# Kernel optimization log

Measured on AMD Instinct MI355X. Metric: run time of the kernel, lower is better.

## Reference

```python
import jax, jax.numpy as jnp
import numpy as np

B, D, N, H = 2, 1024, 2048, 16
DH = D // H  # head dim 64


def setup_inputs() -> dict:
    key = jax.random.key(0)
    ks = jax.random.split(key, 10)
    query = jax.random.normal(ks[0], (B, D, N), jnp.float32)
    att_mask = jax.random.randint(ks[1], (B, 1, N), 0, 2).astype(bool)
    w = lambda k: jax.random.normal(k, (D, D), jnp.float32) * 0.02
    b = lambda k: jax.random.normal(k, (D,), jnp.float32) * 0.02
    return dict(
        query=query,
        Wq=w(ks[2]), bq=b(ks[3]),
        Wk=w(ks[4]), bk=b(ks[5]),
        Wv=w(ks[6]), bv=b(ks[7]),
        Wo=w(ks[8]), bo=b(ks[9]),
        att_mask=att_mask,
    )


def _proj(W, bias, x):  # conv1d k=1: [B,D,N] -> [B,D,N]
    return jnp.einsum('ed,bdn->ben', W, x) + bias[None, :, None]


def _split_heads(t):  # [B,N,D] -> [B*H,N,DH], batch-major flatten
    return t.reshape(B, N, H, DH).transpose(0, 2, 1, 3).reshape(B * H, N, DH)


def _attention(q, k, v, att_mask):
    scale = 1.0 / np.sqrt(DH)
    att = jnp.einsum('bqd,bkd->bqk', q * scale, k)  # [B*H,N,N]
    # faithful to original: mask repeated along q_len then tiled num_heads times on dim 0
    m = jnp.tile(jnp.broadcast_to(att_mask, (B, N, N)), (H, 1, 1))
    att = jnp.where(m, att, -jnp.inf)
    fully_masked = ~m.any(axis=(-2, -1))  # [B*H]
    att = jnp.where(fully_masked[:, None, None], 1e-5, att)
    p = jax.nn.softmax(att, axis=-1)
    y = jnp.einsum('bqk,bkd->bqd', p, v)
    return y * (~fully_masked).astype(y.dtype)[:, None, None]


def reference(query, Wq, bq, Wk, bk, Wv, bv, Wo, bo, att_mask):
    # projections (Conv1d kernel_size=1 == channel-dim linear)
    q = _split_heads(_proj(Wq, bq, query).transpose(0, 2, 1))
    k = _split_heads(_proj(Wk, bk, query).transpose(0, 2, 1))
    v = _split_heads(_proj(Wv, bv, query).transpose(0, 2, 1))
    y = _attention(q, k, v, att_mask)  # [B*H,N,DH]
    # combine heads -> [B,N,D] -> channels-first [B,D,N]
    z = y.reshape(B, H, N, DH).transpose(0, 2, 1, 3).reshape(B, N, D).transpose(0, 2, 1)
    # output projection (dropouts are identity in eval mode)
    return _proj(Wo, bo, z)
```

## Files before the change

kernel.cpp:

```cpp
#include <hip/hip_runtime.h>
#include <hip/hip_bf16.h>

#define BATCH 2
#define DMODEL 1024
#define SEQ 2048
#define NHEAD 16
#define DHEAD 64
#define BH (BATCH*NHEAD)
#define COLS (BATCH*SEQ)

typedef __attribute__((ext_vector_type(8))) short bf16x8;
typedef __attribute__((ext_vector_type(4))) float f32x4;
typedef __attribute__((ext_vector_type(16))) float f32x16;

__device__ inline unsigned short f2bf(float f) {
    unsigned u = __builtin_bit_cast(unsigned, f);
    unsigned r = (u + 0x7FFFu + ((u >> 16) & 1u)) >> 16;
    return (unsigned short)r;
}

__device__ inline f32x4 mfma16(bf16x8 a, bf16x8 b, f32x4 c) {
    return __builtin_amdgcn_mfma_f32_16x16x32_bf16(a, b, c, 0, 0, 0);
}
__device__ inline f32x16 mfma32(bf16x8 a, bf16x8 b, f32x16 c) {
    return __builtin_amdgcn_mfma_f32_32x32x16_bf16(a, b, c, 0, 0, 0);
}

__device__ __forceinline__ void gload_lds16(const unsigned short* g, unsigned short* l) {
    __builtin_amdgcn_global_load_lds(
        (const __attribute__((address_space(1))) unsigned int*)g,
        (__attribute__((address_space(3))) unsigned int*)l, 16, 0, 0);
}

__device__ inline unsigned cvtpk(float lo, float hi) {
    unsigned r;
    asm("v_cvt_pk_bf16_f32 %0, %1, %2" : "=v"(r) : "v"(lo), "v"(hi));
    return r;
}
__device__ inline float fexp2(float x) {
    float r;
    asm("v_exp_f32 %0, %1" : "=v"(r) : "v"(x));
    return r;
}

__global__ __launch_bounds__(256) void cvt_w(
    const float* __restrict__ w0, const float* __restrict__ w1,
    const float* __restrict__ w2, const float* __restrict__ w3,
    unsigned short* __restrict__ out)
{
    int which = blockIdx.y;
    const float* src = (which == 0) ? w0 : (which == 1) ? w1 : (which == 2) ? w2 : w3;
    size_t base = (size_t)which * (DMODEL * DMODEL);
    size_t i = ((size_t)blockIdx.x * 256 + threadIdx.x) * 4;
    float4 v = *(const float4*)&src[i];
    ushort4 o;
    o.x = f2bf(v.x); o.y = f2bf(v.y); o.z = f2bf(v.z); o.w = f2bf(v.w);
    *(ushort4*)&out[base + i] = o;
}

__global__ __launch_bounds__(64) void prep_mask(
    const int* __restrict__ mask, unsigned long long* __restrict__ mw)
{
    int lane = threadIdx.x;
    int tile = blockIdx.x;
    int mb = tile >> 5, tt = tile & 31;
    unsigned long long bits = __ballot(mask[mb * SEQ + tt * 64 + lane] != 0);
    if (lane == 0) mw[tile] = bits;
}

__global__ __launch_bounds__(256) void transpose_q(
    const float* __restrict__ q, unsigned short* __restrict__ Xt)
{
    __shared__ float tile[32][33];
    int b = blockIdx.z;
    int d0 = blockIdx.y * 32, n0 = blockIdx.x * 32;
    int tx = threadIdx.x, ty = threadIdx.y;
#pragma unroll
    for (int i = 0; i < 32; i += 8)
        tile[ty + i][tx] = q[(size_t)b * DMODEL * SEQ + (size_t)(d0 + ty + i) * SEQ + n0 + tx];
    __syncthreads();
#pragma unroll
    for (int i = 0; i < 32; i += 8)
        Xt[(size_t)b * SEQ * DMODEL + (size_t)(n0 + ty + i) * DMODEL + d0 + tx] = f2bf(tile[tx][ty + i]);
}

__global__ __launch_bounds__(256) void gemm_qkv(
    const unsigned short* __restrict__ Xt,
    const unsigned short* __restrict__ W3,
    const float* __restrict__ bq, const float* __restrict__ bk, const float* __restrict__ bv,
    unsigned short* __restrict__ Qb, unsigned short* __restrict__ Kbuf,
    unsigned short* __restrict__ Vtb)
{
    const int K = DMODEL;
    __shared__ unsigned short sA[128 * 32];
    __shared__ unsigned short sB[128 * 32];
    int t = threadIdx.x, lane = t & 63, w = t >> 6;
    int wr = w >> 1, wc = w & 1;
    int tt0 = blockIdx.y * 128;
    int ct0 = blockIdx.x * 128;
    int mat = ct0 >> 10, ec0 = ct0 & 1023;
    const float* bs = (mat == 0) ? bq : (mat == 1) ? bk : bv;
    int rl = lane & 15, ko = (lane >> 4) << 3;
    int srow = lane >> 2, scol = (lane & 3) << 3;

    f32x4 acc[4][4] = {};
    for (int kb = 0; kb < K; kb += 32) {
        __syncthreads();
        gload_lds16(&Xt[(size_t)(tt0 + w * 32 + srow) * K + kb + scol],      &sA[(w * 32) * 32]);
        gload_lds16(&Xt[(size_t)(tt0 + w * 32 + 16 + srow) * K + kb + scol], &sA[(w * 32 + 16) * 32]);
        gload_lds16(&W3[(size_t)(ct0 + w * 32 + srow) * K + kb + scol],      &sB[(w * 32) * 32]);
        gload_lds16(&W3[(size_t)(ct0 + w * 32 + 16 + srow) * K + kb + scol], &sB[(w * 32 + 16) * 32]);
        __syncthreads();
        bf16x8 af[4], bfr[4];
#pragma unroll
        for (int m = 0; m < 4; m++)
            af[m] = *(const bf16x8*)&sA[(wr * 64 + m * 16 + rl) * 32 + ko];
#pragma unroll
        for (int n = 0; n < 4; n++)
            bfr[n] = *(const bf16x8*)&sB[(wc * 64 + n * 16 + rl) * 32 + ko];
#pragma unroll
        for (int m = 0; m < 4; m++)
#pragma unroll
            for (int n = 0; n < 4; n++)
                acc[m][n] = mfma16(af[m], bfr[n], acc[m][n]);
    }

    const float QS = 0.125f;
    int rowb = (lane >> 4) * 4, col = lane & 15;
#pragma unroll
    for (int m = 0; m < 4; m++) {
#pragma unroll
        for (int n = 0; n < 4; n++) {
            int ee = ec0 + wc * 64 + n * 16 + col;
            int hh = ee >> 6, dd = ee & 63;
            float bias = bs[ee];
#pragma unroll
            for (int r = 0; r < 4; r++) {
                int tk = tt0 + wr * 64 + m * 16 + rowb + r;
                int b = tk >> 11, nn = tk & (SEQ - 1);
                float v = acc[m][n][r] + bias;
                if (mat == 0) {
                    v *= QS;
                    Qb[((size_t)(b * NHEAD + hh) * SEQ + nn) * DHEAD + dd] = f2bf(v);
                } else if (mat == 1) {
                    Kbuf[((size_t)(b * NHEAD + hh) * SEQ + nn) * DHEAD + dd] = f2bf(v);
                } else {
                    int q2 = (nn >> 2) & 3;
                    int q2s = ((q2 & 1) << 1) | (q2 >> 1);
                    int np = (nn & ~15) | (q2s << 2) | (nn & 3);
                    Vtb[((size_t)(b * NHEAD + hh) * DHEAD + dd) * SEQ + np] = f2bf(v);
                }
            }
        }
    }
}

__global__ __launch_bounds__(256) void gemm_out(
    const unsigned short* __restrict__ A,
    const unsigned short* __restrict__ Bt,
    const float* __restrict__ bias,
    float* __restrict__ outf)
{
    const int K = DMODEL;
    __shared__ unsigned short sA[128 * 32];
    __shared__ unsigned short sB[64 * 32];
    int t = threadIdx.x, lane = t & 63, w = t >> 6;
    int wr = w >> 1, wc = w & 1;
    int et0 = blockIdx.y * 128, ct0 = blockIdx.x * 64;
    int rl = lane & 15, ko = (lane >> 4) << 3;
    int srow = lane >> 2, scol = (lane & 3) << 3;

    f32x4 acc[4][2] = {};
    for (int kb = 0; kb < K; kb += 32) {
        __syncthreads();
        gload_lds16(&A[(size_t)(et0 + w * 16 + srow) * K + kb + scol],      &sA[(w * 16) * 32]);
        gload_lds16(&A[(size_t)(et0 + 64 + w * 16 + srow) * K + kb + scol], &sA[(64 + w * 16) * 32]);
        gload_lds16(&Bt[(size_t)(ct0 + w * 16 + srow) * K + kb + scol],     &sB[(w * 16) * 32]);
        __syncthreads();
        bf16x8 af[4], bfr[2];
#pragma unroll
        for (int m = 0; m < 4; m++)
            af[m] = *(const bf16x8*)&sA[(wr * 64 + m * 16 + rl) * 32 + ko];
#pragma unroll
        for (int n = 0; n < 2; n++)
            bfr[n] = *(const bf16x8*)&sB[(wc * 32 + n * 16 + rl) * 32 + ko];
#pragma unroll
        for (int m = 0; m < 4; m++)
#pragma unroll
            for (int n = 0; n < 2; n++)
                acc[m][n] = mfma16(af[m], bfr[n], acc[m][n]);
    }

    int rowb = (lane >> 4) * 4, col = lane & 15;
#pragma unroll
    for (int m = 0; m < 4; m++) {
#pragma unroll
        for (int n = 0; n < 2; n++) {
            int c = ct0 + wc * 32 + n * 16 + col;
            int b = c >> 11, nn = c & (SEQ - 1);
#pragma unroll
            for (int r = 0; r < 4; r++) {
                int e = et0 + wr * 64 + m * 16 + rowb + r;
                outf[((size_t)b * DMODEL + e) * SEQ + nn] = acc[m][n][r] + bias[e];
            }
        }
    }
}

__global__ __launch_bounds__(256, 2) void attn(
    const unsigned short* __restrict__ Q,
    const unsigned short* __restrict__ Kb,
    const unsigned short* __restrict__ Vt,
    const unsigned long long* __restrict__ mwords,
    unsigned short* __restrict__ Zt)
{
    __shared__ unsigned short sK[2][64 * 64];
    __shared__ unsigned short sV[2][64 * 64];

    int bid = blockIdx.x;
    int xcd = bid & 7, slot = bid >> 3;
    int bh = xcd + 8 * (slot >> 4);
    int qb = slot & 15;
    int b = bh >> 4, h = bh & 15;
    int mb = bh & (BATCH - 1);
    int t = threadIdx.x, lane = t & 63, w = t >> 6;
    int hi = lane >> 5, ql = lane & 31;
    int q0 = qb * 128 + w * 32;
    const unsigned short* Qp = Q + (size_t)bh * SEQ * DHEAD;
    const unsigned short* Kp = Kb + (size_t)bh * SEQ * DHEAD;
    const unsigned short* Vp = Vt + (size_t)bh * DHEAD * SEQ;
    const unsigned long long* mw = mwords + mb * 32;

    int srow0 = w * 16 + (lane >> 3);
    int ssw   = ((lane & 7) ^ ((lane >> 3) & 7)) << 3;

    unsigned long long anyb = 0ull;
#pragma unroll
    for (int i = 0; i < 32; i++) anyb |= mw[i];

    bf16x8 qf[4];
#pragma unroll
    for (int c = 0; c < 4; c++)
        qf[c] = *(const bf16x8*)&Qp[(size_t)(q0 + ql) * DHEAD + c * 16 + hi * 8];

    f32x16 Y0 = {}, Y1 = {};
    float m_ = -1e30f, l_ = 0.f;
    const float LOG2E = 1.442695041f;

    int rsw = ql & 7;

    {
        int k0 = 0;
        gload_lds16(&Kp[(size_t)(k0 + srow0) * DHEAD + ssw],     &sK[0][(w * 16) * 64]);
        gload_lds16(&Kp[(size_t)(k0 + srow0 + 8) * DHEAD + ssw], &sK[0][(w * 16 + 8) * 64]);
        gload_lds16(&Vp[(size_t)srow0 * SEQ + k0 + ssw],         &sV[0][(w * 16) * 64]);
        gload_lds16(&Vp[(size_t)(srow0 + 8) * SEQ + k0 + ssw],   &sV[0][(w * 16 + 8) * 64]);
    }
    __syncthreads();

    for (int tt0 = 0; tt0 < 32; tt0++) {
        int cur = tt0 & 1;
        if (tt0 < 31) {
            int kn = (tt0 + 1) * 64;
            gload_lds16(&Kp[(size_t)(kn + srow0) * DHEAD + ssw],     &sK[cur ^ 1][(w * 16) * 64]);
            gload_lds16(&Kp[(size_t)(kn + srow0 + 8) * DHEAD + ssw], &sK[cur ^ 1][(w * 16 + 8) * 64]);
            gload_lds16(&Vp[(size_t)srow0 * SEQ + kn + ssw],         &sV[cur ^ 1][(w * 16) * 64]);
            gload_lds16(&Vp[(size_t)(srow0 + 8) * SEQ + kn + ssw],   &sV[cur ^ 1][(w * 16 + 8) * 64]);
        }
        unsigned long long mbits = mw[tt0];

        f32x16 S0 = {}, S1 = {};
        __builtin_amdgcn_s_setprio(1);
#pragma unroll
        for (int c = 0; c < 4; c++) {
            bf16x8 kf = *(const bf16x8*)&sK[cur][ql * 64 + ((((c << 1) | hi) ^ rsw) << 3)];
            S0 = mfma32(kf, qf[c], S0);
        }
#pragma unroll
        for (int c = 0; c < 4; c++) {
            bf16x8 kf = *(const bf16x8*)&sK[cur][(32 + ql) * 64 + ((((c << 1) | hi) ^ rsw) << 3)];
            S1 = mfma32(kf, qf[c], S1);
        }
        __builtin_amdgcn_s_setprio(0);

        float t0[16];
#pragma unroll
        for (int r = 0; r < 16; r++) t0[r] = fmaxf(S0[r], S1[r]);
#pragma unroll
        for (int s = 8; s > 0; s >>= 1)
#pragma unroll
            for (int r = 0; r < 8; r++)
                if (r < s) t0[r] = fmaxf(t0[r], t0[r + s]);
        float pmax = fmaxf(t0[0], __shfl_xor(t0[0], 32, 64));

        float mnew = fmaxf(m_, pmax);
        if (!__all(pmax <= m_ + 8.0f)) {
            float al = __expf(m_ - mnew);
            m_ = mnew;
            l_ *= al;
#pragma unroll
            for (int reg = 0; reg < 16; reg++) {
                float av = __shfl(al, (reg & 3) + 8 * (reg >> 2) + 4 * hi, 64);
                Y0[reg] *= av;
                Y1[reg] *= av;
            }
        }

        unsigned long long msh = mbits >> (hi * 4);
        unsigned w0m = (unsigned)msh, w1m = (unsigned)(msh >> 32);
        float nmL = -m_ * LOG2E;
        float p[32];
        float s4[4] = {0.f, 0.f, 0.f, 0.f};
#pragma unroll
        for (int tt = 0; tt < 2; tt++)
#pragma unroll
            for (int rr = 0; rr < 16; rr++) {
                const int bpos = (rr & 3) + 8 * (rr >> 2);
                unsigned mm = tt ? w1m : w0m;
                unsigned sg = (unsigned)((int)(mm << (31 - bpos)) >> 31);
                float s = tt ? S1[rr] : S0[rr];
                float e = fexp2(fmaf(s, LOG2E, nmL));
                e = __builtin_bit_cast(float, __builtin_bit_cast(unsigned, e) & sg);
                p[tt * 16 + rr] = e;
                s4[rr & 3] += e;
            }
        float sm = (s4[0] + s4[1]) + (s4[2] + s4[3]);
        sm += __shfl_xor(sm, 32, 64);
        l_ += sm;

        unsigned PKa[8], PKb[8];
#pragma unroll
        for (int i = 0; i < 8; i++) {
            PKa[i] = cvtpk(p[4 * i], p[4 * i + 1]);
            PKb[i] = cvtpk(p[4 * i + 2], p[4 * i + 3]);
        }

        bf16x8 pa[4];
#pragma unroll
        for (int ks = 0; ks < 4; ks++) {
            union { unsigned u[4]; bf16x8 v; } pu;
            pu.u[0] = PKa[2 * ks];
            pu.u[1] = PKb[2 * ks];
            pu.u[2] = PKa[2 * ks + 1];
            pu.u[3] = PKb[2 * ks + 1];
            pa[ks] = pu.v;
        }

        __builtin_amdgcn_s_setprio(1);
#pragma unroll
        for (int ks = 0; ks < 4; ks++) {
            bf16x8 vb0 = *(const bf16x8*)&sV[cur][ql * 64 + ((((ks << 1) | hi) ^ rsw) << 3)];
            bf16x8 vb1 = *(const bf16x8*)&sV[cur][(32 + ql) * 64 + ((((ks << 1) | hi) ^ rsw) << 3)];
            Y0 = mfma32(pa[ks], vb0, Y0);
            Y1 = mfma32(pa[ks], vb1, Y1);
        }
        __builtin_amdgcn_s_setprio(0);

        __syncthreads();
    }

    float linv = (anyb != 0ull) ? (1.0f / l_) : 0.f;
#pragma unroll
    for (int reg = 0; reg < 16; reg++) {
        int row = (reg & 3) + 8 * (reg >> 2) + 4 * hi;
        float lv = __shfl(linv, row, 64);
        int n = q0 + row;
        size_t base = ((size_t)b * SEQ + n) * DMODEL + h * DHEAD;
        Zt[base + ql] = f2bf(Y0[reg] * lv);
        Zt[base + 32 + ql] = f2bf(Y1[reg] * lv);
    }
}

extern "C" void kernel_launch(void* const* d_in, const int* in_sizes, int n_in,
                              void* d_out, int out_size, void* d_ws, size_t ws_size,
                              hipStream_t stream) {
    const float* query = (const float*)d_in[0];
    const float* Wq = (const float*)d_in[1];
    const float* bq = (const float*)d_in[2];
    const float* Wk = (const float*)d_in[3];
    const float* bk = (const float*)d_in[4];
    const float* Wv = (const float*)d_in[5];
    const float* bv = (const float*)d_in[6];
    const float* Wo = (const float*)d_in[7];
    const float* bo = (const float*)d_in[8];
    const int* mask = (const int*)d_in[9];
    float* out = (float*)d_out;

    char* ws = (char*)d_ws;
    unsigned short* Wb  = (unsigned short*)(ws);
    unsigned short* Xt  = (unsigned short*)(ws + ((size_t)8  << 20));
    unsigned short* Qb  = (unsigned short*)(ws + ((size_t)16 << 20));
    unsigned short* Kbuf= (unsigned short*)(ws + ((size_t)24 << 20));
    unsigned short* Vtb = (unsigned short*)(ws + ((size_t)32 << 20));
    unsigned short* Zt  = (unsigned short*)(ws + ((size_t)40 << 20));
    unsigned long long* mwords = (unsigned long long*)(ws + ((size_t)48 << 20));

    const size_t WSZ = (size_t)DMODEL * DMODEL;

    cvt_w<<<dim3(DMODEL * DMODEL / 1024, 4), 256, 0, stream>>>(Wq, Wk, Wv, Wo, Wb);
    prep_mask<<<64, 64, 0, stream>>>(mask, mwords);
    transpose_q<<<dim3(SEQ / 32, DMODEL / 32, BATCH), dim3(32, 8), 0, stream>>>(query, Xt);

    gemm_qkv<<<dim3(3 * DMODEL / 128, COLS / 128), 256, 0, stream>>>(
        Xt, Wb, bq, bk, bv, Qb, Kbuf, Vtb);

    attn<<<512, 256, 0, stream>>>(Qb, Kbuf, Vtb, mwords, Zt);

    gemm_out<<<dim3(COLS / 64, DMODEL / 128), 256, 0, stream>>>(
        Wb + 3 * WSZ, Zt, bo, out);
}
```

Measured before the change: 139.1 us.

## Fold key mask into V and compute softmax denominator with an extra MFMA

Masked keys are now zeroed in V during the QKV projection, and a bf16 mask vector (1.0 or 0) is added as an extra B operand. The softmax row sum is then accumulated by a third MFMA against this vector instead of per-element bit masking, adds and cross-lane shuffles. This removes the per-score mask select and sum reduction from the attention inner loop. In exchange it adds one MFMA and one global load per k-step, and the denominator is now accumulated from bf16-rounded probabilities rather than fp32 ones.

```diff
diff --git a/kernel.cpp b/kernel.cpp
--- a/kernel.cpp
+++ b/kernel.cpp
@@ -59,13 +59,19 @@
 }
 
 __global__ __launch_bounds__(64) void prep_mask(
-    const int* __restrict__ mask, unsigned long long* __restrict__ mw)
+    const int* __restrict__ mask, unsigned long long* __restrict__ mw,
+    unsigned short* __restrict__ maskvb)
 {
     int lane = threadIdx.x;
     int tile = blockIdx.x;
     int mb = tile >> 5, tt = tile & 31;
-    unsigned long long bits = __ballot(mask[mb * SEQ + tt * 64 + lane] != 0);
+    int mv = mask[mb * SEQ + tt * 64 + lane];
+    unsigned long long bits = __ballot(mv != 0);
     if (lane == 0) mw[tile] = bits;
+    int q2 = (lane >> 2) & 3;
+    int q2s = ((q2 & 1) << 1) | (q2 >> 1);
+    int pp = (lane & ~15) | (q2s << 2) | (lane & 3);
+    maskvb[mb * SEQ + tt * 64 + pp] = mv ? 0x3F80 : 0;
 }
 
 __global__ __launch_bounds__(256) void transpose_q(
@@ -88,6 +94,7 @@
     const unsigned short* __restrict__ Xt,
     const unsigned short* __restrict__ W3,
     const float* __restrict__ bq, const float* __restrict__ bk, const float* __restrict__ bv,
+    const int* __restrict__ mask,
     unsigned short* __restrict__ Qb, unsigned short* __restrict__ Kbuf,
     unsigned short* __restrict__ Vtb)
 {
@@ -145,6 +152,7 @@
                 } else if (mat == 1) {
                     Kbuf[((size_t)(b * NHEAD + hh) * SEQ + nn) * DHEAD + dd] = f2bf(v);
                 } else {
+                    if (mask[(hh & 1) * SEQ + nn] == 0) v = 0.f;
                     int q2 = (nn >> 2) & 3;
                     int q2s = ((q2 & 1) << 1) | (q2 >> 1);
                     int np = (nn & ~15) | (q2s << 2) | (nn & 3);
@@ -212,6 +220,7 @@
     const unsigned short* __restrict__ Kb,
     const unsigned short* __restrict__ Vt,
     const unsigned long long* __restrict__ mwords,
+    const unsigned short* __restrict__ maskvb,
     unsigned short* __restrict__ Zt)
 {
     __shared__ unsigned short sK[2][64 * 64];
@@ -230,6 +239,7 @@
     const unsigned short* Kp = Kb + (size_t)bh * SEQ * DHEAD;
     const unsigned short* Vp = Vt + (size_t)bh * DHEAD * SEQ;
     const unsigned long long* mw = mwords + mb * 32;
+    const unsigned short* Mv = maskvb + mb * SEQ;
 
     int srow0 = w * 16 + (lane >> 3);
     int ssw   = ((lane & 7) ^ ((lane >> 3) & 7)) << 3;
@@ -243,18 +253,17 @@
     for (int c = 0; c < 4; c++)
         qf[c] = *(const bf16x8*)&Qp[(size_t)(q0 + ql) * DHEAD + c * 16 + hi * 8];
 
-    f32x16 Y0 = {}, Y1 = {};
-    float m_ = -1e30f, l_ = 0.f;
+    f32x16 Y0 = {}, Y1 = {}, Yl = {};
+    float m_ = -1e30f;
     const float LOG2E = 1.442695041f;
 
     int rsw = ql & 7;
 
     {
-        int k0 = 0;
-        gload_lds16(&Kp[(size_t)(k0 + srow0) * DHEAD + ssw],     &sK[0][(w * 16) * 64]);
-        gload_lds16(&Kp[(size_t)(k0 + srow0 + 8) * DHEAD + ssw], &sK[0][(w * 16 + 8) * 64]);
-        gload_lds16(&Vp[(size_t)srow0 * SEQ + k0 + ssw],         &sV[0][(w * 16) * 64]);
-        gload_lds16(&Vp[(size_t)(srow0 + 8) * SEQ + k0 + ssw],   &sV[0][(w * 16 + 8) * 64]);
+        gload_lds16(&Kp[(size_t)srow0 * DHEAD + ssw],           &sK[0][(w * 16) * 64]);
+        gload_lds16(&Kp[(size_t)(srow0 + 8) * DHEAD + ssw],     &sK[0][(w * 16 + 8) * 64]);
+        gload_lds16(&Vp[(size_t)srow0 * SEQ + ssw],             &sV[0][(w * 16) * 64]);
+        gload_lds16(&Vp[(size_t)(srow0 + 8) * SEQ + ssw],       &sV[0][(w * 16 + 8) * 64]);
     }
     __syncthreads();
 
@@ -267,7 +276,6 @@
             gload_lds16(&Vp[(size_t)srow0 * SEQ + kn + ssw],         &sV[cur ^ 1][(w * 16) * 64]);
             gload_lds16(&Vp[(size_t)(srow0 + 8) * SEQ + kn + ssw],   &sV[cur ^ 1][(w * 16 + 8) * 64]);
         }
-        unsigned long long mbits = mw[tt0];
 
         f32x16 S0 = {}, S1 = {};
         __builtin_amdgcn_s_setprio(1);
@@ -297,36 +305,21 @@
         if (!__all(pmax <= m_ + 8.0f)) {
             float al = __expf(m_ - mnew);
             m_ = mnew;
-            l_ *= al;
 #pragma unroll
             for (int reg = 0; reg < 16; reg++) {
                 float av = __shfl(al, (reg & 3) + 8 * (reg >> 2) + 4 * hi, 64);
                 Y0[reg] *= av;
                 Y1[reg] *= av;
+                Yl[reg] *= av;
             }
         }
 
-        unsigned long long msh = mbits >> (hi * 4);
-        unsigned w0m = (unsigned)msh, w1m = (unsigned)(msh >> 32);
         float nmL = -m_ * LOG2E;
         float p[32];
-        float s4[4] = {0.f, 0.f, 0.f, 0.f};
-#pragma unroll
-        for (int tt = 0; tt < 2; tt++)
-#pragma unroll
-            for (int rr = 0; rr < 16; rr++) {
-                const int bpos = (rr & 3) + 8 * (rr >> 2);
-                unsigned mm = tt ? w1m : w0m;
-                unsigned sg = (unsigned)((int)(mm << (31 - bpos)) >> 31);
-                float s = tt ? S1[rr] : S0[rr];
-                float e = fexp2(fmaf(s, LOG2E, nmL));
-                e = __builtin_bit_cast(float, __builtin_bit_cast(unsigned, e) & sg);
-                p[tt * 16 + rr] = e;
-                s4[rr & 3] += e;
-            }
-        float sm = (s4[0] + s4[1]) + (s4[2] + s4[3]);
-        sm += __shfl_xor(sm, 32, 64);
-        l_ += sm;
+#pragma unroll
+        for (int rr = 0; rr < 16; rr++) p[rr] = fexp2(fmaf(S0[rr], LOG2E, nmL));
+#pragma unroll
+        for (int rr = 0; rr < 16; rr++) p[16 + rr] = fexp2(fmaf(S1[rr], LOG2E, nmL));
 
         unsigned PKa[8], PKb[8];
 #pragma unroll
@@ -351,19 +344,20 @@
         for (int ks = 0; ks < 4; ks++) {
             bf16x8 vb0 = *(const bf16x8*)&sV[cur][ql * 64 + ((((ks << 1) | hi) ^ rsw) << 3)];
             bf16x8 vb1 = *(const bf16x8*)&sV[cur][(32 + ql) * 64 + ((((ks << 1) | hi) ^ rsw) << 3)];
+            bf16x8 im  = *(const bf16x8*)&Mv[tt0 * 64 + 16 * ks + 8 * hi];
             Y0 = mfma32(pa[ks], vb0, Y0);
             Y1 = mfma32(pa[ks], vb1, Y1);
+            Yl = mfma32(pa[ks], im,  Yl);
         }
         __builtin_amdgcn_s_setprio(0);
 
         __syncthreads();
     }
 
-    float linv = (anyb != 0ull) ? (1.0f / l_) : 0.f;
 #pragma unroll
     for (int reg = 0; reg < 16; reg++) {
+        float lv = (anyb != 0ull) ? (1.0f / Yl[reg]) : 0.f;
         int row = (reg & 3) + 8 * (reg >> 2) + 4 * hi;
-        float lv = __shfl(linv, row, 64);
         int n = q0 + row;
         size_t base = ((size_t)b * SEQ + n) * DMODEL + h * DHEAD;
         Zt[base + ql] = f2bf(Y0[reg] * lv);
@@ -394,17 +388,18 @@
     unsigned short* Vtb = (unsigned short*)(ws + ((size_t)32 << 20));
     unsigned short* Zt  = (unsigned short*)(ws + ((size_t)40 << 20));
     unsigned long long* mwords = (unsigned long long*)(ws + ((size_t)48 << 20));
+    unsigned short* maskvb = (unsigned short*)(ws + ((size_t)48 << 20) + 65536);
 
     const size_t WSZ = (size_t)DMODEL * DMODEL;
 
     cvt_w<<<dim3(DMODEL * DMODEL / 1024, 4), 256, 0, stream>>>(Wq, Wk, Wv, Wo, Wb);
-    prep_mask<<<64, 64, 0, stream>>>(mask, mwords);
+    prep_mask<<<64, 64, 0, stream>>>(mask, mwords, maskvb);
     transpose_q<<<dim3(SEQ / 32, DMODEL / 32, BATCH), dim3(32, 8), 0, stream>>>(query, Xt);
 
     gemm_qkv<<<dim3(3 * DMODEL / 128, COLS / 128), 256, 0, stream>>>(
-        Xt, Wb, bq, bk, bv, Qb, Kbuf, Vtb);
-
-    attn<<<512, 256, 0, stream>>>(Qb, Kbuf, Vtb, mwords, Zt);
+        Xt, Wb, bq, bk, bv, mask, Qb, Kbuf, Vtb);
+
+    attn<<<512, 256, 0, stream>>>(Qb, Kbuf, Vtb, mwords, maskvb, Zt);
 
     gemm_out<<<dim3(COLS / 64, DMODEL / 128), 256, 0, stream>>>(
         Wb + 3 * WSZ, Zt, bo, out);
```

Measured after the change: 138.9 us. Within noise of the previous version (-0.2%).
